# Optimization experiments

Hardware: AMD Instinct MI355X
Metric: run time of the kernel (lower is better)

Reference implementation:

```python
import jax, jax.numpy as jnp
import numpy as np

EMB = 128
HID = 64
B = 4096
H = 200


def setup_inputs() -> dict:
    key = jax.random.key(0)
    ks = jax.random.split(key, 9)
    historical_embs = jax.random.normal(ks[0], (B, H, EMB), dtype=jnp.float32)
    candidate_emb = jax.random.normal(ks[1], (B, EMB), dtype=jnp.float32)
    mask = jax.random.randint(ks[2], (B, H), 0, 2, dtype=jnp.int32)
    # attention_net params: Linear(2*EMB -> HID), Linear(HID -> HID//2), Linear(HID//2 -> 1)
    def init_linear(k, fan_in, fan_out):
        k1, k2 = jax.random.split(k)
        bound = 1.0 / np.sqrt(fan_in)
        W = jax.random.uniform(k1, (fan_in, fan_out), jnp.float32, -bound, bound)
        b = jax.random.uniform(k2, (fan_out,), jnp.float32, -bound, bound)
        return W, b
    W1, b1 = init_linear(ks[3], 2 * EMB, HID)
    W2, b2 = init_linear(ks[4], HID, HID // 2)
    W3, b3 = init_linear(ks[5], HID // 2, 1)
    return {
        "historical_embs": historical_embs,
        "candidate_emb": candidate_emb,
        "W1": W1, "b1": b1, "W2": W2, "b2": b2, "W3": W3, "b3": b3,
        "mask": mask,
    }


def reference(historical_embs, candidate_emb, W1, b1, W2, b2, W3, b3, mask):
    # [B, H, 2*EMB] concat of history and broadcast candidate
    num_history = historical_embs.shape[1]
    cand = jnp.broadcast_to(candidate_emb[:, None, :], historical_embs.shape)
    combined = jnp.concatenate([historical_embs, cand], axis=-1)
    h = jax.nn.relu(combined @ W1 + b1)          # [B, H, HID]
    h = jax.nn.relu(h @ W2 + b2)                 # [B, H, HID//2]
    scores = (h @ W3 + b3)[..., 0]               # [B, H]
    scores = scores + (1.0 - mask.astype(scores.dtype)) * -1e9
    attention_weights = jax.nn.softmax(scores, axis=1)  # [B, H]
    aggregated = jnp.einsum('bh,bhd->bd', attention_weights, historical_embs)
    return aggregated, attention_weights
```

## Files before the change

kernel.cpp:

```cpp
#include <hip/hip_runtime.h>

#define EMB  128
#define HID  64
#define NH   200
#define BT   256
#define LDX  132
#define LDH1 68

typedef _Float16 half_t;
typedef half_t half2v __attribute__((ext_vector_type(2)));
typedef half_t half4v __attribute__((ext_vector_type(4)));
typedef half_t half8v __attribute__((ext_vector_type(8)));
typedef float  f32x4  __attribute__((ext_vector_type(4)));

__global__ __launch_bounds__(BT, 2) void attn_agg_kernel(
    const float* __restrict__ hist,
    const float* __restrict__ cand,
    const float* __restrict__ W1,
    const float* __restrict__ b1,
    const float* __restrict__ W2,
    const float* __restrict__ b2,
    const float* __restrict__ W3,
    const float* __restrict__ b3,
    const int*   __restrict__ mask,
    float* __restrict__ out_agg,
    float* __restrict__ out_attn)
{
    __shared__ __align__(16) half_t X_s[NH * LDX];
    __shared__ __align__(16) half_t H1_s[NH * LDH1];
    __shared__ float c1_s[HID];
    __shared__ float attn_s[NH];

    const int b    = blockIdx.x;
    const int tid  = threadIdx.x;
    const int lane = tid & 63;
    const int wid  = tid >> 6;
    const int c16  = lane & 15;
    const int quad = lane >> 4;

    const float* hb = hist + (size_t)b * (NH * EMB);

    half8v w1f[4];
    #pragma unroll
    for (int ks = 0; ks < 4; ++ks)
        #pragma unroll
        for (int j = 0; j < 8; ++j)
            w1f[ks][j] = (half_t)W1[(ks * 32 + quad * 8 + j) * HID + wid * 16 + c16];

    half8v w2f[2][2];
    #pragma unroll
    for (int nt = 0; nt < 2; ++nt)
        #pragma unroll
        for (int ks = 0; ks < 2; ++ks)
            #pragma unroll
            for (int j = 0; j < 8; ++j)
                w2f[nt][ks][j] = (half_t)W2[(ks * 32 + quad * 8 + j) * (HID / 2) + nt * 16 + c16];

    const float w3a = W3[c16];
    const float w3b = W3[16 + c16];
    const float bb2a = b2[c16];
    const float bb2b = b2[16 + c16];

    {
        const float4* src = (const float4*)hb;
        #pragma unroll 5
        for (int t = 0; t < 25; ++t) {
            int i = t * BT + tid;
            int h = i >> 5, c4 = i & 31;
            float4 v = src[i];
            half2v p0 = {(half_t)v.x, (half_t)v.y};
            half2v p1 = {(half_t)v.z, (half_t)v.w};
            *(half2v*)&X_s[h * LDX + c4 * 4]     = p0;
            *(half2v*)&X_s[h * LDX + c4 * 4 + 2] = p1;
        }
    }

    if (tid < HID) {
        const float* cb = cand + (size_t)b * EMB;
        float acc = b1[tid];
        #pragma unroll 8
        for (int k = 0; k < EMB; ++k)
            acc = fmaf(cb[k], W1[(EMB + k) * HID + tid], acc);
        c1_s[tid] = acc;
    }
    __syncthreads();

    {
        const float c1v = c1_s[wid * 16 + c16];
        for (int t = 0; t < 13; ++t) {
            const int m0 = (t < 12) ? t * 16 : 184;
            const int row = m0 + c16;
            f32x4 acc = {0.f, 0.f, 0.f, 0.f};
            #pragma unroll
            for (int ks = 0; ks < 4; ++ks) {
                const half_t* ap = &X_s[row * LDX + ks * 32 + quad * 8];
                half4v alo = *(const half4v*)ap;
                half4v ahi = *(const half4v*)(ap + 4);
                half8v a = __builtin_shufflevector(alo, ahi, 0, 1, 2, 3, 4, 5, 6, 7);
                acc = __builtin_amdgcn_mfma_f32_16x16x32_f16(a, w1f[ks], acc, 0, 0, 0);
            }
            #pragma unroll
            for (int i = 0; i < 4; ++i) {
                int r = m0 + 4 * quad + i;
                float hv = fmaxf(acc[i] + c1v, 0.f);
                H1_s[r * LDH1 + wid * 16 + c16] = (half_t)hv;
            }
        }
    }
    __syncthreads();

    for (int t = wid; t < 13; t += 4) {
        const int m0 = (t < 12) ? t * 16 : 184;
        const int row = m0 + c16;
        f32x4 acc0 = {0.f, 0.f, 0.f, 0.f};
        f32x4 acc1 = {0.f, 0.f, 0.f, 0.f};
        #pragma unroll
        for (int ks = 0; ks < 2; ++ks) {
            const half_t* ap = &H1_s[row * LDH1 + ks * 32 + quad * 8];
            half4v alo = *(const half4v*)ap;
            half4v ahi = *(const half4v*)(ap + 4);
            half8v a = __builtin_shufflevector(alo, ahi, 0, 1, 2, 3, 4, 5, 6, 7);
            acc0 = __builtin_amdgcn_mfma_f32_16x16x32_f16(a, w2f[0][ks], acc0, 0, 0, 0);
            acc1 = __builtin_amdgcn_mfma_f32_16x16x32_f16(a, w2f[1][ks], acc1, 0, 0, 0);
        }
        float sp[4];
        #pragma unroll
        for (int i = 0; i < 4; ++i)
            sp[i] = fmaxf(acc0[i] + bb2a, 0.f) * w3a + fmaxf(acc1[i] + bb2b, 0.f) * w3b;
        #pragma unroll
        for (int m = 1; m < 16; m <<= 1)
            #pragma unroll
            for (int i = 0; i < 4; ++i)
                sp[i] += __shfl_xor(sp[i], m, 64);
        if (c16 == 0) {
            const int lo = (t == 12) ? 192 : m0;
            #pragma unroll
            for (int i = 0; i < 4; ++i) {
                int r = m0 + 4 * quad + i;
                if (r >= lo) attn_s[r] = sp[i];
            }
        }
    }
    __syncthreads();

    if (tid < 64) {
        const int* mb = mask + (size_t)b * NH;
        float s0 = attn_s[tid]       + (1.f - (float)mb[tid])       * -1e9f;
        float s1 = attn_s[64 + tid]  + (1.f - (float)mb[64 + tid])  * -1e9f;
        float s2 = attn_s[128 + tid] + (1.f - (float)mb[128 + tid]) * -1e9f;
        float s3 = (tid < 8) ? attn_s[192 + tid] + (1.f - (float)mb[192 + tid]) * -1e9f : -1e30f;
        float m = fmaxf(fmaxf(s0, s1), fmaxf(s2, s3));
        #pragma unroll
        for (int off = 32; off; off >>= 1) m = fmaxf(m, __shfl_xor(m, off, 64));
        float e0 = __expf(s0 - m);
        float e1 = __expf(s1 - m);
        float e2 = __expf(s2 - m);
        float e3 = (tid < 8) ? __expf(s3 - m) : 0.f;
        float sum = e0 + e1 + e2 + e3;
        #pragma unroll
        for (int off = 32; off; off >>= 1) sum += __shfl_xor(sum, off, 64);
        float inv = 1.f / sum;
        e0 *= inv; e1 *= inv; e2 *= inv; e3 *= inv;
        attn_s[tid] = e0; attn_s[64 + tid] = e1; attn_s[128 + tid] = e2;
        if (tid < 8) attn_s[192 + tid] = e3;
        float* oa = out_attn + (size_t)b * NH;
        oa[tid] = e0; oa[64 + tid] = e1; oa[128 + tid] = e2;
        if (tid < 8) oa[192 + tid] = e3;
    }
    __syncthreads();

    {
        int c = tid & 63;
        int g = wid;
        float2 acc = make_float2(0.f, 0.f);
        for (int h = g * 50; h < g * 50 + 50; ++h) {
            float w = attn_s[h];
            half2v v = *(const half2v*)&X_s[h * LDX + c * 2];
            acc.x = fmaf(w, (float)v[0], acc.x);
            acc.y = fmaf(w, (float)v[1], acc.y);
        }
        __syncthreads();
        float2* red = (float2*)X_s;
        red[g * 64 + c] = acc;
        __syncthreads();
        if (tid < 64) {
            float2 r0 = red[tid], r1 = red[64 + tid], r2 = red[128 + tid], r3 = red[192 + tid];
            float2 o = make_float2(r0.x + r1.x + r2.x + r3.x,
                                   r0.y + r1.y + r2.y + r3.y);
            *(float2*)&out_agg[(size_t)b * EMB + tid * 2] = o;
        }
    }
}

extern "C" void kernel_launch(void* const* d_in, const int* in_sizes, int n_in,
                              void* d_out, int out_size, void* d_ws, size_t ws_size,
                              hipStream_t stream) {
    const float* hist = (const float*)d_in[0];
    const float* cand = (const float*)d_in[1];
    const float* W1   = (const float*)d_in[2];
    const float* b1   = (const float*)d_in[3];
    const float* W2   = (const float*)d_in[4];
    const float* b2   = (const float*)d_in[5];
    const float* W3   = (const float*)d_in[6];
    const float* b3   = (const float*)d_in[7];
    const int*   mask = (const int*)d_in[8];

    const int B = in_sizes[0] / (NH * EMB);
    float* out_agg  = (float*)d_out;
    float* out_attn = out_agg + (size_t)B * EMB;

    attn_agg_kernel<<<B, BT, 0, stream>>>(hist, cand, W1, b1, W2, b2, W3, b3,
                                          mask, out_agg, out_attn);
}
```

Before: 625.2 us.

## Precompute weight fragments and candidate projection in a separate prologue kernel

Adds a precompute kernel that converts W1/W2 into per-thread half-precision MFMA fragments once and computes the candidate projection c1 for four batches per block, writing both to workspace. The main kernel loads the prepacked fragments with vector loads and reads c1 instead of doing strided scalar weight loads and a serial 128-step dot product in every block. This removes redundant per-block work from the main kernel, in exchange for an extra launch and a workspace round trip. It assumes B is divisible by 4 and that the workspace is large enough.

```diff
diff --git a/kernel.cpp b/kernel.cpp
--- a/kernel.cpp
+++ b/kernel.cpp
@@ -7,21 +7,61 @@
 #define LDX  132
 #define LDH1 68
 
+#define WS_FRAG_BYTES 32768
+
 typedef _Float16 half_t;
 typedef half_t half2v __attribute__((ext_vector_type(2)));
 typedef half_t half4v __attribute__((ext_vector_type(4)));
 typedef half_t half8v __attribute__((ext_vector_type(8)));
 typedef float  f32x4  __attribute__((ext_vector_type(4)));
 
+__global__ __launch_bounds__(BT) void precomp_kernel(
+    const float* __restrict__ W1, const float* __restrict__ b1,
+    const float* __restrict__ W2, const float* __restrict__ cand,
+    half8v* __restrict__ frag_ws, float* __restrict__ c1_ws, int nblk_c1)
+{
+    const int tid = threadIdx.x;
+    if ((int)blockIdx.x == nblk_c1) {
+        const int lane = tid & 63, wid = tid >> 6;
+        const int c16 = lane & 15, quad = lane >> 4;
+        half8v f[8];
+        #pragma unroll
+        for (int ks = 0; ks < 4; ++ks)
+            #pragma unroll
+            for (int j = 0; j < 8; ++j)
+                f[ks][j] = (half_t)W1[(ks * 32 + quad * 8 + j) * HID + wid * 16 + c16];
+        #pragma unroll
+        for (int nt = 0; nt < 2; ++nt)
+            #pragma unroll
+            for (int ks = 0; ks < 2; ++ks)
+                #pragma unroll
+                for (int j = 0; j < 8; ++j)
+                    f[4 + nt * 2 + ks][j] =
+                        (half_t)W2[(ks * 32 + quad * 8 + j) * (HID / 2) + nt * 16 + c16];
+        #pragma unroll
+        for (int i = 0; i < 8; ++i) frag_ws[tid * 8 + i] = f[i];
+    } else {
+        __shared__ float W1b_s[EMB * HID];
+        __shared__ float cand_s[4 * EMB];
+        const int b0 = blockIdx.x * 4;
+        for (int i = tid; i < EMB * HID; i += BT) W1b_s[i] = W1[EMB * HID + i];
+        for (int i = tid; i < 4 * EMB; i += BT) cand_s[i] = cand[(size_t)b0 * EMB + i];
+        __syncthreads();
+        const int bl = tid >> 6, j = tid & 63;
+        float acc = b1[j];
+        #pragma unroll 8
+        for (int k = 0; k < EMB; ++k)
+            acc = fmaf(cand_s[bl * EMB + k], W1b_s[k * HID + j], acc);
+        c1_ws[(size_t)(b0 + bl) * HID + j] = acc;
+    }
+}
+
 __global__ __launch_bounds__(BT, 2) void attn_agg_kernel(
     const float* __restrict__ hist,
-    const float* __restrict__ cand,
-    const float* __restrict__ W1,
-    const float* __restrict__ b1,
-    const float* __restrict__ W2,
+    const half8v* __restrict__ frag_ws,
+    const float* __restrict__ c1_ws,
     const float* __restrict__ b2,
     const float* __restrict__ W3,
-    const float* __restrict__ b3,
     const int*   __restrict__ mask,
     float* __restrict__ out_agg,
     float* __restrict__ out_attn)
@@ -40,26 +80,18 @@
 
     const float* hb = hist + (size_t)b * (NH * EMB);
 
+    const half8v* fw = frag_ws + tid * 8;
     half8v w1f[4];
-    #pragma unroll
-    for (int ks = 0; ks < 4; ++ks)
-        #pragma unroll
-        for (int j = 0; j < 8; ++j)
-            w1f[ks][j] = (half_t)W1[(ks * 32 + quad * 8 + j) * HID + wid * 16 + c16];
-
+    w1f[0] = fw[0]; w1f[1] = fw[1]; w1f[2] = fw[2]; w1f[3] = fw[3];
     half8v w2f[2][2];
-    #pragma unroll
-    for (int nt = 0; nt < 2; ++nt)
-        #pragma unroll
-        for (int ks = 0; ks < 2; ++ks)
-            #pragma unroll
-            for (int j = 0; j < 8; ++j)
-                w2f[nt][ks][j] = (half_t)W2[(ks * 32 + quad * 8 + j) * (HID / 2) + nt * 16 + c16];
-
-    const float w3a = W3[c16];
-    const float w3b = W3[16 + c16];
+    w2f[0][0] = fw[4]; w2f[0][1] = fw[5]; w2f[1][0] = fw[6]; w2f[1][1] = fw[7];
+
+    const float w3a  = W3[c16];
+    const float w3b  = W3[16 + c16];
     const float bb2a = b2[c16];
     const float bb2b = b2[16 + c16];
+
+    if (tid < HID) c1_s[tid] = c1_ws[(size_t)b * HID + tid];
 
     {
         const float4* src = (const float4*)hb;
@@ -74,15 +106,6 @@
             *(half2v*)&X_s[h * LDX + c4 * 4 + 2] = p1;
         }
     }
-
-    if (tid < HID) {
-        const float* cb = cand + (size_t)b * EMB;
-        float acc = b1[tid];
-        #pragma unroll 8
-        for (int k = 0; k < EMB; ++k)
-            acc = fmaf(cb[k], W1[(EMB + k) * HID + tid], acc);
-        c1_s[tid] = acc;
-    }
     __syncthreads();
 
     {
@@ -202,13 +225,17 @@
     const float* W2   = (const float*)d_in[4];
     const float* b2   = (const float*)d_in[5];
     const float* W3   = (const float*)d_in[6];
-    const float* b3   = (const float*)d_in[7];
     const int*   mask = (const int*)d_in[8];
 
     const int B = in_sizes[0] / (NH * EMB);
     float* out_agg  = (float*)d_out;
     float* out_attn = out_agg + (size_t)B * EMB;
 
-    attn_agg_kernel<<<B, BT, 0, stream>>>(hist, cand, W1, b1, W2, b2, W3, b3,
-                                          mask, out_agg, out_attn);
+    half8v* frag_ws = (half8v*)d_ws;
+    float*  c1_ws   = (float*)((char*)d_ws + WS_FRAG_BYTES);
+
+    const int nblk_c1 = B / 4;
+    precomp_kernel<<<nblk_c1 + 1, BT, 0, stream>>>(W1, b1, W2, cand, frag_ws, c1_ws, nblk_c1);
+    attn_agg_kernel<<<B, BT, 0, stream>>>(hist, frag_ws, c1_ws, b2, W3, mask,
+                                          out_agg, out_attn);
 }
```

New measurement: 572.7 us. -8.4%, faster.
